# Kernel tuning notes

Measured on AMD Instinct MI355X. Metric: run time of the kernel, lower is better.

The kernel has to match this reference:

```python
import jax, jax.numpy as jnp
import numpy as np
import math

B, S, IN, D, H = 128, 128, 16, 256, 256


def _gates(pre):
    i, f, g, o = jnp.split(pre, 4, axis=-1)
    return jax.nn.sigmoid(i), jax.nn.sigmoid(f), jnp.tanh(g), jax.nn.sigmoid(o)


def _lstm_dir(xp, Whh):
    # xp: [B,S,4H] precomputed input projection (+ both biases); scan over time.
    b = xp.shape[0]
    h_dim = Whh.shape[1]

    def step(carry, xt):
        h, c = carry
        i, f, g, o = _gates(xt + h @ Whh.T)
        c = f * c + i * g
        h = o * jnp.tanh(c)
        return (h, c), h

    init = (jnp.zeros((b, h_dim), xp.dtype), jnp.zeros((b, h_dim), xp.dtype))
    (hT, cT), hs = jax.lax.scan(step, init, jnp.swapaxes(xp, 0, 1))
    return jnp.swapaxes(hs, 0, 1), hT, cT


def _layernorm(x, g, b, eps=1e-5):
    m = jnp.mean(x, -1, keepdims=True)
    v = jnp.mean((x - m) ** 2, -1, keepdims=True)
    return (x - m) * jax.lax.rsqrt(v + eps) * g + b


def _forward(x, proj_W, proj_b, ln_g, ln_b,
             Wih_f, Whh_f, bih_f, bhh_f,
             Wih_b, Whh_b, bih_b, bhh_b,
             Wih_d, Whh_d, bih_d, bhh_d,
             hb_W, hb_b, cb_W, cb_b,
             gW1, gW2, gv, pW1, pW2, pv):
    b, s, _ = x.shape
    h_dim = Whh_d.shape[1]
    # Projector: Linear -> Tanh -> LayerNorm
    emb = _layernorm(jnp.tanh(x @ proj_W.T + proj_b), ln_g, ln_b)  # [B,S,D]
    # Bidirectional LSTM encoder (PyTorch gate order i,f,g,o)
    hf, hTf, cTf = _lstm_dir(emb @ Wih_f.T + (bih_f + bhh_f), Whh_f)
    hb_rev, hTb, cTb = _lstm_dir((emb @ Wih_b.T + (bih_b + bhh_b))[:, ::-1], Whh_b)
    hb_out = hb_rev[:, ::-1]
    enc = jnp.concatenate([hf, hb_out], -1)  # [B,S,2H]
    # Bridges to decoder init state
    h = jnp.tanh(jnp.concatenate([hTf, hTb], -1) @ hb_W.T + hb_b)
    c = jnp.tanh(jnp.concatenate([cTf, cTb], -1) @ cb_W.T + cb_b)
    dec_in = jnp.mean(enc, axis=1)  # [B,2H]
    # W1(encoder_outputs) is step-invariant: precompute once for both attentions
    g_ref = enc @ gW1.T  # [B,S,H]
    p_ref = enc @ pW1.T  # [B,S,H]
    scale = 1.0 / math.sqrt(h_dim)
    mask0 = jnp.zeros((b, s), jnp.bool_)

    def step(carry, _):
        h, c, mask, dec_in = carry
        # LSTMCell
        i, f, g, o = _gates(dec_in @ Wih_d.T + h @ Whh_d.T + bih_d + bhh_d)
        c = f * c + i * g
        h = o * jnp.tanh(c)
        # glimpse attention
        gs = jnp.tanh(g_ref + (h @ gW2.T)[:, None, :]) @ gv * scale  # [B,S]
        gp = jax.nn.softmax(jnp.where(mask, -1e9, gs), axis=1)
        ctx = jnp.einsum('bs,bsh->bh', gp, enc)  # [B,2H]
        # pointer attention (query = h + context[:, :H])
        ps = jnp.tanh(p_ref + ((h + ctx[:, :h_dim]) @ pW2.T)[:, None, :]) @ pv * scale
        ps = jnp.where(mask, -1e9, ps)  # masked scores are the returned logits
        sel = jnp.argmax(ps, axis=1)  # argmax(softmax(ps)) == argmax(ps)
        mask = mask | jax.nn.one_hot(sel, s, dtype=jnp.bool_)
        dec_in = jnp.take_along_axis(enc, sel[:, None, None], axis=1)[:, 0]
        return (h, c, mask, dec_in), (ps, sel)

    _, (logits, ptrs) = jax.lax.scan(step, (h, c, mask0, dec_in), None, length=s)
    return jnp.swapaxes(logits, 0, 1), jnp.swapaxes(ptrs, 0, 1)


def setup_inputs() -> dict:
    key = jax.random.key(0)
    ks = iter(jax.random.split(key, 20))

    def w(*shape):
        return jax.random.normal(next(ks), shape, jnp.float32) * 0.05

    z = lambda *shape: jnp.zeros(shape, jnp.float32)
    return {
        'x': jax.random.normal(next(ks), (B, S, IN), jnp.float32),
        'proj_W': w(D, IN), 'proj_b': z(D), 'ln_g': jnp.ones((D,), jnp.float32), 'ln_b': z(D),
        'Wih_f': w(4 * H, D), 'Whh_f': w(4 * H, H), 'bih_f': z(4 * H), 'bhh_f': z(4 * H),
        'Wih_b': w(4 * H, D), 'Whh_b': w(4 * H, H), 'bih_b': z(4 * H), 'bhh_b': z(4 * H),
        'Wih_d': w(4 * H, 2 * H), 'Whh_d': w(4 * H, H), 'bih_d': z(4 * H), 'bhh_d': z(4 * H),
        'hb_W': w(H, 2 * H), 'hb_b': z(H), 'cb_W': w(H, 2 * H), 'cb_b': z(H),
        'gW1': w(H, 2 * H), 'gW2': w(H, H), 'gv': w(H),
        'pW1': w(H, 2 * H), 'pW2': w(H, H), 'pv': w(H),
    }


def reference(x, proj_W, proj_b, ln_g, ln_b, Wih_f, Whh_f, bih_f, bhh_f, Wih_b, Whh_b, bih_b, bhh_b, Wih_d, Whh_d, bih_d, bhh_d, hb_W, hb_b, cb_W, cb_b, gW1, gW2, gv, pW1, pW2, pv):
    return _forward(x, proj_W, proj_b, ln_g, ln_b, Wih_f, Whh_f, bih_f, bhh_f, Wih_b, Whh_b, bih_b, bhh_b, Wih_d, Whh_d, bih_d, bhh_d, hb_W, hb_b, cb_W, cb_b, gW1, gW2, gv, pW1, pW2, pv)
```

## Files before the change

kernel.cpp:

```cpp
#include <hip/hip_runtime.h>
#include <cstdint>
#include <cstddef>

#define DEVINL __device__ __forceinline__

typedef float f32x4 __attribute__((ext_vector_type(4)));

DEVINL float ntload1(const float* p) {
    return __builtin_nontemporal_load(p);
}
DEVINL f32x4 ld4(const float* p) {
    return *reinterpret_cast<const f32x4*>(p);
}

DEVINL float frcp(float x) { return __builtin_amdgcn_rcpf(x); }
DEVINL float ftanh_fast(float x) {
    float e = __expf(2.0f * x);
    return 1.0f - 2.0f * frcp(e + 1.0f);
}
DEVINL float sig_precise(float x) { return 1.0f / (1.0f + expf(-x)); }
DEVINL float tanh_precise(float x) { return tanhf(x); }

#define BB 128
#define SS 128
#define IND 16
#define DD 256
#define HH 256
#define H4 1024
#define H2 512

__global__ __launch_bounds__(256) void k_proj_ln(
    const float* __restrict__ x, const float* __restrict__ projW,
    const float* __restrict__ projB, const float* __restrict__ ln_g,
    const float* __restrict__ ln_b, float* __restrict__ emb)
{
    __shared__ float Wl[256 * 17];
    __shared__ float xl[16];
    __shared__ float red[256];
    const int row = blockIdx.x;
    const int tid = threadIdx.x;
    for (int idx = tid; idx < 256 * 16; idx += 256) {
        int d = idx >> 4, i = idx & 15;
        Wl[d * 17 + i] = projW[idx];
    }
    if (tid < 16) xl[tid] = x[row * 16 + tid];
    __syncthreads();
    float acc = projB[tid];
#pragma unroll
    for (int i = 0; i < 16; ++i) acc = fmaf(Wl[tid * 17 + i], xl[i], acc);
    float v = tanh_precise(acc);
    red[tid] = v;
    __syncthreads();
    for (int s2 = 128; s2 > 0; s2 >>= 1) { if (tid < s2) red[tid] += red[tid + s2]; __syncthreads(); }
    float mean = red[0] * (1.0f / 256.0f);
    __syncthreads();
    float dlt = v - mean;
    red[tid] = dlt * dlt;
    __syncthreads();
    for (int s2 = 128; s2 > 0; s2 >>= 1) { if (tid < s2) red[tid] += red[tid + s2]; __syncthreads(); }
    float var = red[0] * (1.0f / 256.0f);
    float rs = 1.0f / sqrtf(var + 1e-5f);
    emb[(size_t)row * 256 + tid] = dlt * rs * ln_g[tid] + ln_b[tid];
}

__global__ __launch_bounds__(256) void k_gemm_nt(
    const float* __restrict__ A, int lda,
    const float* __restrict__ Bm,
    float* __restrict__ C,
    int M, int N, int K,
    const float* __restrict__ bias1, const float* __restrict__ bias2,
    int flags)
{
    __shared__ __align__(16) float As[16][132];
    __shared__ __align__(16) float Bs[16][132];
    const int tid = threadIdx.x;
    const int m0 = blockIdx.x * 128;
    const int n0 = blockIdx.y * 128;
    const int r = tid >> 1, half = tid & 1;
    const int tm = tid & 15, tn = tid >> 4;
    float acc[8][8];
#pragma unroll
    for (int i = 0; i < 8; ++i)
#pragma unroll
        for (int j = 0; j < 8; ++j) acc[i][j] = 0.0f;

    for (int k0 = 0; k0 < K; k0 += 16) {
        const float4* pa = reinterpret_cast<const float4*>(&A[(size_t)(m0 + r) * lda + k0 + half * 8]);
        float4 a0 = pa[0], a1 = pa[1];
        const float4* pb = reinterpret_cast<const float4*>(&Bm[(size_t)(n0 + r) * K + k0 + half * 8]);
        float4 b0 = pb[0], b1 = pb[1];
        __syncthreads();
        const int kb = half * 8;
        As[kb + 0][r] = a0.x; As[kb + 1][r] = a0.y; As[kb + 2][r] = a0.z; As[kb + 3][r] = a0.w;
        As[kb + 4][r] = a1.x; As[kb + 5][r] = a1.y; As[kb + 6][r] = a1.z; As[kb + 7][r] = a1.w;
        Bs[kb + 0][r] = b0.x; Bs[kb + 1][r] = b0.y; Bs[kb + 2][r] = b0.z; Bs[kb + 3][r] = b0.w;
        Bs[kb + 4][r] = b1.x; Bs[kb + 5][r] = b1.y; Bs[kb + 6][r] = b1.z; Bs[kb + 7][r] = b1.w;
        __syncthreads();
#pragma unroll
        for (int kk = 0; kk < 16; ++kk) {
            const float4 xa0 = *reinterpret_cast<const float4*>(&As[kk][tm * 8]);
            const float4 xa1 = *reinterpret_cast<const float4*>(&As[kk][tm * 8 + 4]);
            const float4 xb0 = *reinterpret_cast<const float4*>(&Bs[kk][tn * 8]);
            const float4 xb1 = *reinterpret_cast<const float4*>(&Bs[kk][tn * 8 + 4]);
            const float av[8] = {xa0.x, xa0.y, xa0.z, xa0.w, xa1.x, xa1.y, xa1.z, xa1.w};
            const float bv[8] = {xb0.x, xb0.y, xb0.z, xb0.w, xb1.x, xb1.y, xb1.z, xb1.w};
#pragma unroll
            for (int i = 0; i < 8; ++i)
#pragma unroll
                for (int j = 0; j < 8; ++j) acc[i][j] = fmaf(av[i], bv[j], acc[i][j]);
        }
    }
    const int nb = n0 + tn * 8;
    float bias[8];
#pragma unroll
    for (int j = 0; j < 8; ++j) {
        float bbv = 0.0f;
        if (bias1) bbv += bias1[nb + j];
        if (bias2) bbv += bias2[nb + j];
        bias[j] = bbv;
    }
#pragma unroll
    for (int i = 0; i < 8; ++i) {
        const size_t m = (size_t)(m0 + tm * 8 + i);
        float o[8];
#pragma unroll
        for (int j = 0; j < 8; ++j) {
            float vv = acc[i][j] + bias[j];
            if (flags & 1) vv = tanh_precise(vv);
            o[j] = vv;
        }
        float4* pc = reinterpret_cast<float4*>(&C[m * N + nb]);
        pc[0] = make_float4(o[0], o[1], o[2], o[3]);
        pc[1] = make_float4(o[4], o[5], o[6], o[7]);
    }
}

__global__ __launch_bounds__(1024) void k_lstm(
    const float* __restrict__ Whh_f, const float* __restrict__ Whh_b,
    const float* __restrict__ xf, const float* __restrict__ xb,
    float* __restrict__ enc, float* __restrict__ hT, float* __restrict__ cT)
{
    const int wg = blockIdx.x;
    const int dir = wg >> 7;
    const int bat = wg & 127;
    const float* W = dir ? Whh_b : Whh_f;
    const float* xin = dir ? xb : xf;
    const int tid = threadIdx.x;
    const int oct = tid & 7, jg = tid >> 3;

    __shared__ __align__(16) float h_lds[256];
    __shared__ float pre_lds[1024];

    if (tid < 256) h_lds[tid] = 0.0f;
    float c_reg = 0.0f;
    __syncthreads();

    for (int t = 0; t < SS; ++t) {
        const int st = dir ? (SS - 1 - t) : t;
        float hreg[32];
#pragma unroll
        for (int i = 0; i < 8; ++i) {
            f32x4 v = ld4(&h_lds[i * 32 + oct * 4]);
            hreg[i * 4 + 0] = v.x; hreg[i * 4 + 1] = v.y;
            hreg[i * 4 + 2] = v.z; hreg[i * 4 + 3] = v.w;
        }
        {
            f32x4 wA[8], wB[8];
            {
                const float* bp = &W[(size_t)jg * 256 + oct * 4];
#pragma unroll
                for (int i = 0; i < 8; ++i) wA[i] = ld4(bp + i * 32);
            }
            auto wstep = [&](f32x4 (&cur)[8], f32x4 (&nxt)[8], int q) {
                if (q < 7) {
                    const float* bp = &W[(size_t)((q + 1) * 128 + jg) * 256 + oct * 4];
#pragma unroll
                    for (int i = 0; i < 8; ++i) nxt[i] = ld4(bp + i * 32);
                }
                float a0 = 0.0f;
#pragma unroll
                for (int i = 0; i < 8; ++i) {
                    a0 = fmaf(cur[i].x, hreg[i * 4 + 0], a0);
                    a0 = fmaf(cur[i].y, hreg[i * 4 + 1], a0);
                    a0 = fmaf(cur[i].z, hreg[i * 4 + 2], a0);
                    a0 = fmaf(cur[i].w, hreg[i * 4 + 3], a0);
                }
                a0 += __shfl_xor(a0, 1); a0 += __shfl_xor(a0, 2); a0 += __shfl_xor(a0, 4);
                if (oct == 0) pre_lds[q * 128 + jg] = a0;
            };
#pragma unroll 1
            for (int q = 0; q < 8; q += 2) { wstep(wA, wB, q); wstep(wB, wA, q + 1); }
        }
        __syncthreads();
        if (tid < 256) {
            const int gc = tid;
            const float* xrow = &xin[((size_t)bat * SS + st) * 1024];
            float pi = pre_lds[gc]       + ntload1(&xrow[gc]);
            float pf = pre_lds[256 + gc] + ntload1(&xrow[256 + gc]);
            float pg = pre_lds[512 + gc] + ntload1(&xrow[512 + gc]);
            float po = pre_lds[768 + gc] + ntload1(&xrow[768 + gc]);
            float ig = sig_precise(pi), fg = sig_precise(pf);
            float gg = tanh_precise(pg), og = sig_precise(po);
            float cn = fmaf(fg, c_reg, ig * gg);
            float hn = og * tanh_precise(cn);
            c_reg = cn;
            h_lds[gc] = hn;
            enc[((size_t)bat * SS + st) * 512 + dir * 256 + gc] = hn;
            if (t == SS - 1) {
                hT[(size_t)bat * 512 + dir * 256 + gc] = hn;
                cT[(size_t)bat * 512 + dir * 256 + gc] = cn;
            }
        }
        __syncthreads();
    }
}

__global__ __launch_bounds__(256) void k_meanw(const float* __restrict__ encW, float* __restrict__ pre0)
{
    const int b = blockIdx.x;
    const int tid = threadIdx.x;
    const float4* base = reinterpret_cast<const float4*>(&encW[(size_t)b * SS * 1024]);
    float sx = 0.0f, sy = 0.0f, sz = 0.0f, sw = 0.0f;
    for (int s = 0; s < SS; ++s) {
        float4 v = base[s * 256 + tid];
        sx += v.x; sy += v.y; sz += v.z; sw += v.w;
    }
    float4* out = reinterpret_cast<float4*>(&pre0[(size_t)b * 1024]);
    out[tid] = make_float4(sx * (1.0f / 128.0f), sy * (1.0f / 128.0f), sz * (1.0f / 128.0f), sw * (1.0f / 128.0f));
}

__global__ __launch_bounds__(1024) void k_decoder(
    const float* __restrict__ Whh_d,
    const float* __restrict__ gW2, const float* __restrict__ pW2,
    const float* __restrict__ gv, const float* __restrict__ pv,
    const float* __restrict__ g_ref, const float* __restrict__ p_ref,
    const float* __restrict__ encP, const float* __restrict__ encW,
    const float* __restrict__ pre0, const float* __restrict__ h0,
    const float* __restrict__ c0,
    float* __restrict__ out_logits, float* __restrict__ out_ptrs)
{
    const int b = blockIdx.x;
    const int tid = threadIdx.x;
    const int oct = tid & 7, jg = tid >> 3;
    const int wid = tid >> 6, lane = tid & 63;

    __shared__ __align__(16) float h_lds[256];
    __shared__ float c_lds[256];
    __shared__ float wacc_lds[1024];
    __shared__ float row_lds[1024];
    __shared__ __align__(16) float hgp[512];
    __shared__ __align__(16) float hp_lds[256];
    __shared__ __align__(16) float gv_lds[256];
    __shared__ __align__(16) float pv_lds[256];
    __shared__ float sc_arr[128];
    __shared__ float e_arr[128];
    __shared__ __align__(16) float hp_half[16][256];
    __shared__ int mask_lds[128];
    __shared__ int ulist[128];
    __shared__ int ucount_s;
    __shared__ float Z_s;
    __shared__ int sel_s;

    if (tid < 256) {
        gv_lds[tid] = gv[tid];
        pv_lds[tid] = pv[tid];
        h_lds[tid] = h0[(size_t)b * 256 + tid];
        c_lds[tid] = c0[(size_t)b * 256 + tid];
    }
    if (tid < 128) mask_lds[tid] = 0;
    if (tid == 0) sel_s = -1;
    const float* grefb = g_ref + (size_t)b * SS * 256;
    const float* prefb = p_ref + (size_t)b * SS * 256;
    const float* encPb = encP + (size_t)b * SS * 256;
    __syncthreads();

    {
        float hreg0[32];
#pragma unroll
        for (int i = 0; i < 8; ++i) {
            f32x4 v = ld4(&h_lds[i * 32 + oct * 4]);
            hreg0[i * 4 + 0] = v.x; hreg0[i * 4 + 1] = v.y;
            hreg0[i * 4 + 2] = v.z; hreg0[i * 4 + 3] = v.w;
        }
        f32x4 wA[8], wB[8];
        {
            const float* bp = &Whh_d[(size_t)jg * 256 + oct * 4];
#pragma unroll
            for (int i = 0; i < 8; ++i) wA[i] = ld4(bp + i * 32);
        }
        auto pw = [&](f32x4 (&cur)[8], f32x4 (&nxt)[8], int q) {
            if (q < 7) {
                const float* bp = &Whh_d[(size_t)((q + 1) * 128 + jg) * 256 + oct * 4];
#pragma unroll
                for (int i = 0; i < 8; ++i) nxt[i] = ld4(bp + i * 32);
            }
            float a0 = 0.0f;
#pragma unroll
            for (int i = 0; i < 8; ++i) {
                a0 = fmaf(cur[i].x, hreg0[i * 4 + 0], a0);
                a0 = fmaf(cur[i].y, hreg0[i * 4 + 1], a0);
                a0 = fmaf(cur[i].z, hreg0[i * 4 + 2], a0);
                a0 = fmaf(cur[i].w, hreg0[i * 4 + 3], a0);
            }
            a0 += __shfl_xor(a0, 1); a0 += __shfl_xor(a0, 2); a0 += __shfl_xor(a0, 4);
            if (oct == 0) wacc_lds[q * 128 + jg] = a0;
        };
#pragma unroll 1
        for (int q = 0; q < 8; q += 2) { pw(wA, wB, q); pw(wB, wA, q + 1); }
    }
    __syncthreads();

    for (int t = 0; t < SS; ++t) {
        {
            const int sel = sel_s;
            const float* src = (sel < 0) ? &pre0[(size_t)b * 1024]
                                         : &encW[((size_t)(b * SS + sel)) * 1024];
            row_lds[tid] = src[tid];
        }
        if (tid >= 128 && tid < 256) sc_arr[tid - 128] = -1e9f;
        if (tid < 64) {
            const unsigned long long lowmask = (1ull << lane) - 1ull;
            const bool u0 = (mask_lds[lane] == 0);
            const unsigned long long b0m = __ballot(u0);
            if (u0) ulist[__popcll(b0m & lowmask)] = lane;
            const bool u1 = (mask_lds[lane + 64] == 0);
            const unsigned long long b1m = __ballot(u1);
            const int c0 = __popcll(b0m);
            if (u1) ulist[c0 + __popcll(b1m & lowmask)] = lane + 64;
            if (lane == 0) ucount_s = c0 + __popcll(b1m);
        }
        __syncthreads();
        if (tid < 256) {
            const int ch = tid;
            float pi = wacc_lds[ch]       + row_lds[ch];
            float pf = wacc_lds[256 + ch] + row_lds[256 + ch];
            float pg = wacc_lds[512 + ch] + row_lds[512 + ch];
            float po = wacc_lds[768 + ch] + row_lds[768 + ch];
            float ig = sig_precise(pi), fg = sig_precise(pf);
            float gg = tanh_precise(pg), og = sig_precise(po);
            float cn = fmaf(fg, c_lds[ch], ig * gg);
            float hn = og * tanh_precise(cn);
            c_lds[ch] = cn;
            h_lds[ch] = hn;
        }
        __syncthreads();
        float hreg[32];
#pragma unroll
        for (int i = 0; i < 8; ++i) {
            f32x4 v = ld4(&h_lds[i * 32 + oct * 4]);
            hreg[i * 4 + 0] = v.x; hreg[i * 4 + 1] = v.y;
            hreg[i * 4 + 2] = v.z; hreg[i * 4 + 3] = v.w;
        }
        {
            f32x4 wA[8], wB[8];
            {
                const float* bp = &Whh_d[(size_t)jg * 256 + oct * 4];
#pragma unroll
                for (int i = 0; i < 8; ++i) wA[i] = ld4(bp + i * 32);
            }
            auto pm = [&](f32x4 (&cur)[8], f32x4 (&nxt)[8], int q) {
                if (q < 11) {
                    const int qn = q + 1;
                    const float* bp;
                    if (qn < 8) {
                        bp = &Whh_d[(size_t)(qn * 128 + jg) * 256 + oct * 4];
                    } else {
                        const int r2 = (qn - 8) * 128 + jg;
                        bp = (r2 < 256) ? &gW2[(size_t)r2 * 256 + oct * 4]
                                        : &pW2[(size_t)(r2 - 256) * 256 + oct * 4];
                    }
#pragma unroll
                    for (int i = 0; i < 8; ++i) nxt[i] = ld4(bp + i * 32);
                }
                float a0 = 0.0f;
#pragma unroll
                for (int i = 0; i < 8; ++i) {
                    a0 = fmaf(cur[i].x, hreg[i * 4 + 0], a0);
                    a0 = fmaf(cur[i].y, hreg[i * 4 + 1], a0);
                    a0 = fmaf(cur[i].z, hreg[i * 4 + 2], a0);
                    a0 = fmaf(cur[i].w, hreg[i * 4 + 3], a0);
                }
                a0 += __shfl_xor(a0, 1); a0 += __shfl_xor(a0, 2); a0 += __shfl_xor(a0, 4);
                if (oct == 0) {
                    if (q < 8) wacc_lds[q * 128 + jg] = a0;
                    else       hgp[(q - 8) * 128 + jg] = a0;
                }
            };
#pragma unroll 1
            for (int q = 0; q < 12; q += 2) { pm(wA, wB, q); pm(wB, wA, q + 1); }
        }
        __syncthreads();
        {
            const int uc = ucount_s;
            if (jg < uc) {
                const int r = ulist[jg];
                const float* gr = &grefb[(size_t)r * 256 + oct * 4];
                f32x4 g0[8];
#pragma unroll
                for (int i = 0; i < 8; ++i) g0[i] = ld4(gr + i * 32);
                float part = 0.0f;
#pragma unroll
                for (int i = 0; i < 8; ++i) {
                    const int d = i * 32 + oct * 4;
                    const f32x4 hh = ld4(&hgp[d]);
                    const f32x4 vv = ld4(&gv_lds[d]);
                    part = fmaf(ftanh_fast(g0[i].x + hh.x), vv.x, part);
                    part = fmaf(ftanh_fast(g0[i].y + hh.y), vv.y, part);
                    part = fmaf(ftanh_fast(g0[i].z + hh.z), vv.z, part);
                    part = fmaf(ftanh_fast(g0[i].w + hh.w), vv.w, part);
                }
                part += __shfl_xor(part, 1); part += __shfl_xor(part, 2); part += __shfl_xor(part, 4);
                if (oct == 0) sc_arr[r] = part * 0.0625f;
            }
        }
        __syncthreads();
        if (tid < 64) {
            float s0 = sc_arr[lane], s1 = sc_arr[lane + 64];
            float m = fmaxf(s0, s1);
#pragma unroll
            for (int mk = 1; mk < 64; mk <<= 1) m = fmaxf(m, __shfl_xor(m, mk));
            float e0 = expf(s0 - m), e1 = expf(s1 - m);
            e_arr[lane] = e0; e_arr[lane + 64] = e1;
            float z = e0 + e1;
#pragma unroll
            for (int mk = 1; mk < 64; mk <<= 1) z += __shfl_xor(z, mk);
            if (lane == 0) Z_s = z;
        }
        __syncthreads();
        {
            const int uc = ucount_s;
            const int d4 = lane * 4;
            float ax = 0.0f, ay = 0.0f, az = 0.0f, aw = 0.0f;
            if (wid * 8 < uc) {
                f32x4 p0[8]; float ee[8];
#pragma unroll
                for (int i = 0; i < 8; ++i) {
                    const int k = wid * 8 + i;
                    const int kc = (k < uc) ? k : (uc - 1);
                    const int s = ulist[kc];
                    ee[i] = (k < uc) ? e_arr[s] : 0.0f;
                    p0[i] = ld4(&encPb[(size_t)s * 256 + d4]);
                }
#pragma unroll
                for (int i = 0; i < 8; ++i) {
                    ax = fmaf(p0[i].x, ee[i], ax); ay = fmaf(p0[i].y, ee[i], ay);
                    az = fmaf(p0[i].z, ee[i], az); aw = fmaf(p0[i].w, ee[i], aw);
                }
            }
            *reinterpret_cast<float4*>(&hp_half[wid][d4]) = make_float4(ax, ay, az, aw);
        }
        __syncthreads();
        if (tid < 256) {
            float s = 0.0f;
#pragma unroll
            for (int k = 0; k < 16; ++k) s += hp_half[k][tid];
            hp_lds[tid] = hgp[256 + tid] + s * frcp(Z_s);
        }
        __syncthreads();
        {
            const int uc = ucount_s;
            if (jg < uc) {
                const int r = ulist[jg];
                const float* pr = &prefb[(size_t)r * 256 + oct * 4];
                f32x4 g0[8];
#pragma unroll
                for (int i = 0; i < 8; ++i) g0[i] = ld4(pr + i * 32);
                float part = 0.0f;
#pragma unroll
                for (int i = 0; i < 8; ++i) {
                    const int d = i * 32 + oct * 4;
                    const f32x4 hh = ld4(&hp_lds[d]);
                    const f32x4 vv = ld4(&pv_lds[d]);
                    part = fmaf(ftanh_fast(g0[i].x + hh.x), vv.x, part);
                    part = fmaf(ftanh_fast(g0[i].y + hh.y), vv.y, part);
                    part = fmaf(ftanh_fast(g0[i].z + hh.z), vv.z, part);
                    part = fmaf(ftanh_fast(g0[i].w + hh.w), vv.w, part);
                }
                part += __shfl_xor(part, 1); part += __shfl_xor(part, 2); part += __shfl_xor(part, 4);
                if (oct == 0) sc_arr[r] = part * 0.0625f;
            }
        }
        __syncthreads();
        if (tid < 128) {
            out_logits[((size_t)(b * SS + t)) * SS + tid] = sc_arr[tid];
        }
        if (tid < 64) {
            float v = sc_arr[lane];
            int idx = lane;
            float v2 = sc_arr[lane + 64];
            if (v2 > v) { v = v2; idx = lane + 64; }
#pragma unroll
            for (int mk = 1; mk < 64; mk <<= 1) {
                float ov = __shfl_xor(v, mk);
                int oi = __shfl_xor(idx, mk);
                if (ov > v || (ov == v && oi < idx)) { v = ov; idx = oi; }
            }
            if (lane == 0) {
                sel_s = idx;
                mask_lds[idx] = 1;
                out_ptrs[(size_t)b * SS + t] = (float)idx;
            }
        }
        __syncthreads();
    }
}

extern "C" void kernel_launch(void* const* d_in, const int* in_sizes, int n_in,
                              void* d_out, int out_size, void* d_ws, size_t ws_size,
                              hipStream_t stream)
{
    (void)in_sizes; (void)n_in; (void)out_size; (void)ws_size;
    const float* x      = (const float*)d_in[0];
    const float* proj_W = (const float*)d_in[1];
    const float* proj_b = (const float*)d_in[2];
    const float* ln_g   = (const float*)d_in[3];
    const float* ln_b   = (const float*)d_in[4];
    const float* Wih_f  = (const float*)d_in[5];
    const float* Whh_f  = (const float*)d_in[6];
    const float* bih_f  = (const float*)d_in[7];
    const float* bhh_f  = (const float*)d_in[8];
    const float* Wih_b  = (const float*)d_in[9];
    const float* Whh_b  = (const float*)d_in[10];
    const float* bih_b  = (const float*)d_in[11];
    const float* bhh_b  = (const float*)d_in[12];
    const float* Wih_d  = (const float*)d_in[13];
    const float* Whh_d  = (const float*)d_in[14];
    const float* bih_d  = (const float*)d_in[15];
    const float* bhh_d  = (const float*)d_in[16];
    const float* hb_W   = (const float*)d_in[17];
    const float* hb_b   = (const float*)d_in[18];
    const float* cb_W   = (const float*)d_in[19];
    const float* cb_b   = (const float*)d_in[20];
    const float* gW1    = (const float*)d_in[21];
    const float* gW2    = (const float*)d_in[22];
    const float* gv     = (const float*)d_in[23];
    const float* pW1    = (const float*)d_in[24];
    const float* pW2    = (const float*)d_in[25];
    const float* pv     = (const float*)d_in[26];

    float* ws = (float*)d_ws;
    const size_t o_hT    = 0;
    const size_t o_cT    = 65536;
    const size_t o_h0    = 131072;
    const size_t o_c0    = 163840;
    const size_t o_pre0  = 196608;
    const size_t o_emb   = 0;
    const size_t o_xf    = 4194304;
    const size_t o_xb    = o_xf + 16777216;
    const size_t o_enc   = o_xb + 16777216;
    const size_t o_encW  = o_xf;
    const size_t o_gref  = o_xb;
    const size_t o_pref  = o_xb + 4194304;
    const size_t o_encP  = o_xb + 8388608;

    float* emb  = ws + o_emb;
    float* xf   = ws + o_xf;
    float* xb   = ws + o_xb;
    float* enc  = ws + o_enc;
    float* hT   = ws + o_hT;
    float* cT   = ws + o_cT;
    float* h0b  = ws + o_h0;
    float* c0b  = ws + o_c0;
    float* pre0 = ws + o_pre0;
    float* encW = ws + o_encW;
    float* gref = ws + o_gref;
    float* pref = ws + o_pref;
    float* encP = ws + o_encP;

    float* out_logits = (float*)d_out;
    float* out_ptrs   = out_logits + (size_t)BB * SS * SS;

    k_proj_ln<<<BB * SS, 256, 0, stream>>>(x, proj_W, proj_b, ln_g, ln_b, emb);
    {
        dim3 g(128, 8);
        k_gemm_nt<<<g, 256, 0, stream>>>(emb, 256, Wih_f, xf, 16384, 1024, 256, bih_f, bhh_f, 0);
        k_gemm_nt<<<g, 256, 0, stream>>>(emb, 256, Wih_b, xb, 16384, 1024, 256, bih_b, bhh_b, 0);
    }
    k_lstm<<<256, 1024, 0, stream>>>(Whh_f, Whh_b, xf, xb, enc, hT, cT);
    {
        dim3 g(1, 2);
        k_gemm_nt<<<g, 256, 0, stream>>>(hT, 512, hb_W, h0b, 128, 256, 512, hb_b, nullptr, 1);
        k_gemm_nt<<<g, 256, 0, stream>>>(cT, 512, cb_W, c0b, 128, 256, 512, cb_b, nullptr, 1);
    }
    {
        dim3 g2(128, 2);
        k_gemm_nt<<<g2, 256, 0, stream>>>(enc, 512, gW1, gref, 16384, 256, 512, nullptr, nullptr, 0);
        k_gemm_nt<<<g2, 256, 0, stream>>>(enc, 512, pW1, pref, 16384, 256, 512, nullptr, nullptr, 0);
        dim3 g1(128, 8);
        k_gemm_nt<<<g1, 256, 0, stream>>>(enc, 512, Wih_d, encW, 16384, 1024, 512, bih_d, bhh_d, 0);
        k_gemm_nt<<<g2, 256, 0, stream>>>(enc, 512, pW2, encP, 16384, 256, 256, nullptr, nullptr, 0);
    }
    k_meanw<<<BB, 256, 0, stream>>>(encW, pre0);
    k_decoder<<<128, 1024, 0, stream>>>(Whh_d, gW2, pW2, gv, pv, gref, pref, encP, encW,
                                        pre0, h0b, c0b, out_logits, out_ptrs);
}
```

Baseline: 6.301 ms.

## Split decoder block into attention and Whh-matvec halves; shrink LSTM blocks

The decoder step now gives its first 512 threads the glimpse/pointer attention work, including the W2 projections. The other 512 threads compute the Whh_d·h recurrent matvec in chunks between the existing barriers. Previously the whole block ran the Whh_d matvec plus the W2 projections before attention began, so this overlaps independent work that used to be serialized. The encoder LSTM kernel also moves to 512-thread blocks with two blocks per CU, each thread covering twice as many gate rows. The risk is that attention phases now run on half the threads, and the matvec slices have no prefetch.

```diff
diff --git a/kernel.cpp b/kernel.cpp
--- a/kernel.cpp
+++ b/kernel.cpp
@@ -135,7 +135,7 @@
     }
 }
 
-__global__ __launch_bounds__(1024) void k_lstm(
+__global__ __launch_bounds__(512, 2) void k_lstm(
     const float* __restrict__ Whh_f, const float* __restrict__ Whh_b,
     const float* __restrict__ xf, const float* __restrict__ xb,
     float* __restrict__ enc, float* __restrict__ hT, float* __restrict__ cT)
@@ -172,8 +172,8 @@
                 for (int i = 0; i < 8; ++i) wA[i] = ld4(bp + i * 32);
             }
             auto wstep = [&](f32x4 (&cur)[8], f32x4 (&nxt)[8], int q) {
-                if (q < 7) {
-                    const float* bp = &W[(size_t)((q + 1) * 128 + jg) * 256 + oct * 4];
+                if (q < 15) {
+                    const float* bp = &W[(size_t)((q + 1) * 64 + jg) * 256 + oct * 4];
 #pragma unroll
                     for (int i = 0; i < 8; ++i) nxt[i] = ld4(bp + i * 32);
                 }
@@ -186,10 +186,10 @@
                     a0 = fmaf(cur[i].w, hreg[i * 4 + 3], a0);
                 }
                 a0 += __shfl_xor(a0, 1); a0 += __shfl_xor(a0, 2); a0 += __shfl_xor(a0, 4);
-                if (oct == 0) pre_lds[q * 128 + jg] = a0;
+                if (oct == 0) pre_lds[q * 64 + jg] = a0;
             };
 #pragma unroll 1
-            for (int q = 0; q < 8; q += 2) { wstep(wA, wB, q); wstep(wB, wA, q + 1); }
+            for (int q = 0; q < 16; q += 2) { wstep(wA, wB, q); wstep(wB, wA, q + 1); }
         }
         __syncthreads();
         if (tid < 256) {
@@ -241,8 +241,11 @@
 {
     const int b = blockIdx.x;
     const int tid = threadIdx.x;
-    const int oct = tid & 7, jg = tid >> 3;
+    const int oct = tid & 7;
+    const int jg128 = tid >> 3;
     const int wid = tid >> 6, lane = tid & 63;
+    const int ajg = (tid & 511) >> 3;
+    const int wjg = (tid & 511) >> 3;
 
     __shared__ __align__(16) float h_lds[256];
     __shared__ float c_lds[256];
@@ -254,7 +257,7 @@
     __shared__ __align__(16) float pv_lds[256];
     __shared__ float sc_arr[128];
     __shared__ float e_arr[128];
-    __shared__ __align__(16) float hp_half[16][256];
+    __shared__ __align__(16) float hp_half[8][256];
     __shared__ int mask_lds[128];
     __shared__ int ulist[128];
     __shared__ int ucount_s;
@@ -284,13 +287,13 @@
         }
         f32x4 wA[8], wB[8];
         {
-            const float* bp = &Whh_d[(size_t)jg * 256 + oct * 4];
+            const float* bp = &Whh_d[(size_t)jg128 * 256 + oct * 4];
 #pragma unroll
             for (int i = 0; i < 8; ++i) wA[i] = ld4(bp + i * 32);
         }
         auto pw = [&](f32x4 (&cur)[8], f32x4 (&nxt)[8], int q) {
             if (q < 7) {
-                const float* bp = &Whh_d[(size_t)((q + 1) * 128 + jg) * 256 + oct * 4];
+                const float* bp = &Whh_d[(size_t)((q + 1) * 128 + jg128) * 256 + oct * 4];
 #pragma unroll
                 for (int i = 0; i < 8; ++i) nxt[i] = ld4(bp + i * 32);
             }
@@ -303,7 +306,7 @@
                 a0 = fmaf(cur[i].w, hreg0[i * 4 + 3], a0);
             }
             a0 += __shfl_xor(a0, 1); a0 += __shfl_xor(a0, 2); a0 += __shfl_xor(a0, 4);
-            if (oct == 0) wacc_lds[q * 128 + jg] = a0;
+            if (oct == 0) wacc_lds[q * 128 + jg128] = a0;
         };
 #pragma unroll 1
         for (int q = 0; q < 8; q += 2) { pw(wA, wB, q); pw(wB, wA, q + 1); }
@@ -351,26 +354,35 @@
             hreg[i * 4 + 0] = v.x; hreg[i * 4 + 1] = v.y;
             hreg[i * 4 + 2] = v.z; hreg[i * 4 + 3] = v.w;
         }
-        {
+        auto wround = [&](int q) {
+            const float* bp = &Whh_d[(size_t)(q * 64 + wjg) * 256 + oct * 4];
+            f32x4 w[8];
+#pragma unroll
+            for (int i = 0; i < 8; ++i) w[i] = ld4(bp + i * 32);
+            float a0 = 0.0f;
+#pragma unroll
+            for (int i = 0; i < 8; ++i) {
+                a0 = fmaf(w[i].x, hreg[i * 4 + 0], a0);
+                a0 = fmaf(w[i].y, hreg[i * 4 + 1], a0);
+                a0 = fmaf(w[i].z, hreg[i * 4 + 2], a0);
+                a0 = fmaf(w[i].w, hreg[i * 4 + 3], a0);
+            }
+            a0 += __shfl_xor(a0, 1); a0 += __shfl_xor(a0, 2); a0 += __shfl_xor(a0, 4);
+            if (oct == 0) wacc_lds[q * 64 + wjg] = a0;
+        };
+        if (tid < 512) {
             f32x4 wA[8], wB[8];
             {
-                const float* bp = &Whh_d[(size_t)jg * 256 + oct * 4];
-#pragma unroll
-                for (int i = 0; i < 8; ++i) wA[i] = ld4(bp + i * 32);
-            }
-            auto pm = [&](f32x4 (&cur)[8], f32x4 (&nxt)[8], int q) {
-                if (q < 11) {
-                    const int qn = q + 1;
-                    const float* bp;
-                    if (qn < 8) {
-                        bp = &Whh_d[(size_t)(qn * 128 + jg) * 256 + oct * 4];
-                    } else {
-                        const int r2 = (qn - 8) * 128 + jg;
-                        bp = (r2 < 256) ? &gW2[(size_t)r2 * 256 + oct * 4]
-                                        : &pW2[(size_t)(r2 - 256) * 256 + oct * 4];
-                    }
-#pragma unroll
-                    for (int i = 0; i < 8; ++i) nxt[i] = ld4(bp + i * 32);
+                const float* src0 = (ajg < 256) ? &gW2[(size_t)ajg * 256] : &pW2[(size_t)(ajg - 256) * 256];
+#pragma unroll
+                for (int i = 0; i < 8; ++i) wA[i] = ld4(src0 + oct * 4 + i * 32);
+            }
+            auto p3 = [&](f32x4 (&cur)[8], f32x4 (&nxt)[8], int q) {
+                if (q < 7) {
+                    const int r2 = (q + 1) * 64 + ajg;
+                    const float* src = (r2 < 256) ? &gW2[(size_t)r2 * 256] : &pW2[(size_t)(r2 - 256) * 256];
+#pragma unroll
+                    for (int i = 0; i < 8; ++i) nxt[i] = ld4(src + oct * 4 + i * 32);
                 }
                 float a0 = 0.0f;
 #pragma unroll
@@ -381,37 +393,42 @@
                     a0 = fmaf(cur[i].w, hreg[i * 4 + 3], a0);
                 }
                 a0 += __shfl_xor(a0, 1); a0 += __shfl_xor(a0, 2); a0 += __shfl_xor(a0, 4);
-                if (oct == 0) {
-                    if (q < 8) wacc_lds[q * 128 + jg] = a0;
-                    else       hgp[(q - 8) * 128 + jg] = a0;
-                }
+                if (oct == 0) hgp[q * 64 + ajg] = a0;
             };
 #pragma unroll 1
-            for (int q = 0; q < 12; q += 2) { pm(wA, wB, q); pm(wB, wA, q + 1); }
-        }
-        __syncthreads();
-        {
+            for (int q = 0; q < 8; q += 2) { p3(wA, wB, q); p3(wB, wA, q + 1); }
+        } else {
+            wround(0); wround(1); wround(2);
+        }
+        __syncthreads();
+        if (tid < 512) {
             const int uc = ucount_s;
-            if (jg < uc) {
-                const int r = ulist[jg];
-                const float* gr = &grefb[(size_t)r * 256 + oct * 4];
-                f32x4 g0[8];
-#pragma unroll
-                for (int i = 0; i < 8; ++i) g0[i] = ld4(gr + i * 32);
-                float part = 0.0f;
-#pragma unroll
-                for (int i = 0; i < 8; ++i) {
-                    const int d = i * 32 + oct * 4;
-                    const f32x4 hh = ld4(&hgp[d]);
-                    const f32x4 vv = ld4(&gv_lds[d]);
-                    part = fmaf(ftanh_fast(g0[i].x + hh.x), vv.x, part);
-                    part = fmaf(ftanh_fast(g0[i].y + hh.y), vv.y, part);
-                    part = fmaf(ftanh_fast(g0[i].z + hh.z), vv.z, part);
-                    part = fmaf(ftanh_fast(g0[i].w + hh.w), vv.w, part);
+#pragma unroll 1
+            for (int rep = 0; rep < 2; ++rep) {
+                const int k = ajg + rep * 64;
+                if (k < uc) {
+                    const int r = ulist[k];
+                    const float* gr = &grefb[(size_t)r * 256 + oct * 4];
+                    f32x4 g0[8];
+#pragma unroll
+                    for (int i = 0; i < 8; ++i) g0[i] = ld4(gr + i * 32);
+                    float part = 0.0f;
+#pragma unroll
+                    for (int i = 0; i < 8; ++i) {
+                        const int d = i * 32 + oct * 4;
+                        const f32x4 hh = ld4(&hgp[d]);
+                        const f32x4 vv = ld4(&gv_lds[d]);
+                        part = fmaf(ftanh_fast(g0[i].x + hh.x), vv.x, part);
+                        part = fmaf(ftanh_fast(g0[i].y + hh.y), vv.y, part);
+                        part = fmaf(ftanh_fast(g0[i].z + hh.z), vv.z, part);
+                        part = fmaf(ftanh_fast(g0[i].w + hh.w), vv.w, part);
+                    }
+                    part += __shfl_xor(part, 1); part += __shfl_xor(part, 2); part += __shfl_xor(part, 4);
+                    if (oct == 0) sc_arr[r] = part * 0.0625f;
                 }
-                part += __shfl_xor(part, 1); part += __shfl_xor(part, 2); part += __shfl_xor(part, 4);
-                if (oct == 0) sc_arr[r] = part * 0.0625f;
-            }
+            }
+        } else {
+            wround(3); wround(4); wround(5);
         }
         __syncthreads();
         if (tid < 64) {
@@ -425,60 +442,78 @@
 #pragma unroll
             for (int mk = 1; mk < 64; mk <<= 1) z += __shfl_xor(z, mk);
             if (lane == 0) Z_s = z;
-        }
-        __syncthreads();
-        {
+        } else if (tid >= 512) {
+            wround(6); wround(7);
+        }
+        __syncthreads();
+        if (tid < 512) {
             const int uc = ucount_s;
             const int d4 = lane * 4;
             float ax = 0.0f, ay = 0.0f, az = 0.0f, aw = 0.0f;
-            if (wid * 8 < uc) {
-                f32x4 p0[8]; float ee[8];
-#pragma unroll
-                for (int i = 0; i < 8; ++i) {
-                    const int k = wid * 8 + i;
-                    const int kc = (k < uc) ? k : (uc - 1);
-                    const int s = ulist[kc];
-                    ee[i] = (k < uc) ? e_arr[s] : 0.0f;
-                    p0[i] = ld4(&encPb[(size_t)s * 256 + d4]);
+            if (wid * 16 < uc) {
+#pragma unroll 1
+                for (int half = 0; half < 2; ++half) {
+                    const int k0 = wid * 16 + half * 8;
+                    if (k0 < uc) {
+                        f32x4 p0[8]; float ee[8];
+#pragma unroll
+                        for (int i = 0; i < 8; ++i) {
+                            const int k = k0 + i;
+                            const int kc = (k < uc) ? k : (uc - 1);
+                            const int s = ulist[kc];
+                            ee[i] = (k < uc) ? e_arr[s] : 0.0f;
+                            p0[i] = ld4(&encPb[(size_t)s * 256 + d4]);
+                        }
+#pragma unroll
+                        for (int i = 0; i < 8; ++i) {
+                            ax = fmaf(p0[i].x, ee[i], ax); ay = fmaf(p0[i].y, ee[i], ay);
+                            az = fmaf(p0[i].z, ee[i], az); aw = fmaf(p0[i].w, ee[i], aw);
+                        }
+                    }
                 }
-#pragma unroll
-                for (int i = 0; i < 8; ++i) {
-                    ax = fmaf(p0[i].x, ee[i], ax); ay = fmaf(p0[i].y, ee[i], ay);
-                    az = fmaf(p0[i].z, ee[i], az); aw = fmaf(p0[i].w, ee[i], aw);
-                }
             }
             *reinterpret_cast<float4*>(&hp_half[wid][d4]) = make_float4(ax, ay, az, aw);
+        } else {
+            wround(8); wround(9); wround(10);
         }
         __syncthreads();
         if (tid < 256) {
             float s = 0.0f;
 #pragma unroll
-            for (int k = 0; k < 16; ++k) s += hp_half[k][tid];
+            for (int k = 0; k < 8; ++k) s += hp_half[k][tid];
             hp_lds[tid] = hgp[256 + tid] + s * frcp(Z_s);
-        }
-        __syncthreads();
-        {
+        } else if (tid >= 512) {
+            wround(11); wround(12);
+        }
+        __syncthreads();
+        if (tid < 512) {
             const int uc = ucount_s;
-            if (jg < uc) {
-                const int r = ulist[jg];
-                const float* pr = &prefb[(size_t)r * 256 + oct * 4];
-                f32x4 g0[8];
-#pragma unroll
-                for (int i = 0; i < 8; ++i) g0[i] = ld4(pr + i * 32);
-                float part = 0.0f;
-#pragma unroll
-                for (int i = 0; i < 8; ++i) {
-                    const int d = i * 32 + oct * 4;
-                    const f32x4 hh = ld4(&hp_lds[d]);
-                    const f32x4 vv = ld4(&pv_lds[d]);
-                    part = fmaf(ftanh_fast(g0[i].x + hh.x), vv.x, part);
-                    part = fmaf(ftanh_fast(g0[i].y + hh.y), vv.y, part);
-                    part = fmaf(ftanh_fast(g0[i].z + hh.z), vv.z, part);
-                    part = fmaf(ftanh_fast(g0[i].w + hh.w), vv.w, part);
+#pragma unroll 1
+            for (int rep = 0; rep < 2; ++rep) {
+                const int k = ajg + rep * 64;
+                if (k < uc) {
+                    const int r = ulist[k];
+                    const float* pr = &prefb[(size_t)r * 256 + oct * 4];
+                    f32x4 g0[8];
+#pragma unroll
+                    for (int i = 0; i < 8; ++i) g0[i] = ld4(pr + i * 32);
+                    float part = 0.0f;
+#pragma unroll
+                    for (int i = 0; i < 8; ++i) {
+                        const int d = i * 32 + oct * 4;
+                        const f32x4 hh = ld4(&hp_lds[d]);
+                        const f32x4 vv = ld4(&pv_lds[d]);
+                        part = fmaf(ftanh_fast(g0[i].x + hh.x), vv.x, part);
+                        part = fmaf(ftanh_fast(g0[i].y + hh.y), vv.y, part);
+                        part = fmaf(ftanh_fast(g0[i].z + hh.z), vv.z, part);
+                        part = fmaf(ftanh_fast(g0[i].w + hh.w), vv.w, part);
+                    }
+                    part += __shfl_xor(part, 1); part += __shfl_xor(part, 2); part += __shfl_xor(part, 4);
+                    if (oct == 0) sc_arr[r] = part * 0.0625f;
                 }
-                part += __shfl_xor(part, 1); part += __shfl_xor(part, 2); part += __shfl_xor(part, 4);
-                if (oct == 0) sc_arr[r] = part * 0.0625f;
-            }
+            }
+        } else {
+            wround(13); wround(14); wround(15);
         }
         __syncthreads();
         if (tid < 128) {
@@ -576,7 +611,7 @@
         k_gemm_nt<<<g, 256, 0, stream>>>(emb, 256, Wih_f, xf, 16384, 1024, 256, bih_f, bhh_f, 0);
         k_gemm_nt<<<g, 256, 0, stream>>>(emb, 256, Wih_b, xb, 16384, 1024, 256, bih_b, bhh_b, 0);
     }
-    k_lstm<<<256, 1024, 0, stream>>>(Whh_f, Whh_b, xf, xb, enc, hT, cT);
+    k_lstm<<<256, 512, 0, stream>>>(Whh_f, Whh_b, xf, xb, enc, hT, cT);
     {
         dim3 g(1, 2);
         k_gemm_nt<<<g, 256, 0, stream>>>(hT, 512, hb_W, h0b, 128, 256, 512, hb_b, nullptr, 1);
```

New measurement: 5.231 ms. -17.0%, faster.
